# Kernel tuning notes

Hardware: AMD Instinct MI355X
Metric: run time of the kernel (lower is better)

Reference implementation:

```python
import jax, jax.numpy as jnp
import numpy as np
import math

EMSIZE = 512
NX = 2048        # emsize * (layer_id+1), layer_id=3
H = NX // EMSIZE # 4 heads of size EMSIZE (grow_head path)
B, S = 4, 2048
EPS = 1e-5


def _layernorm(x, g, b):
    u = jnp.mean(x, axis=-1, keepdims=True)
    s = jnp.mean((x - u) ** 2, axis=-1, keepdims=True)
    return g * (x - u) / jnp.sqrt(s + EPS) + b


def _gelu(x):
    # OpenAI tanh-approx gelu, exactly as in source
    return 0.5 * x * (1.0 + jnp.tanh(jnp.sqrt(2.0 / jnp.pi) * (x + 0.044715 * x ** 3)))


def setup_inputs() -> dict:
    key = jax.random.key(0)
    ks = jax.random.split(key, 8)
    std = 0.02
    return {
        "x": jax.random.normal(ks[0], (B, S, NX), jnp.float32),
        "w_qkv": jax.random.normal(ks[1], (NX, 3 * NX), jnp.float32) * std,
        "b_qkv": jnp.zeros((3 * NX,), jnp.float32),
        "w_ao": jax.random.normal(ks[2], (NX, NX), jnp.float32) * std,
        "b_ao": jnp.zeros((NX,), jnp.float32),
        "ln1_g": jnp.ones((NX,), jnp.float32),
        "ln1_b": jnp.zeros((NX,), jnp.float32),
        "w_fc": jax.random.normal(ks[3], (NX, 4 * NX), jnp.float32) * std,
        "b_fc": jnp.zeros((4 * NX,), jnp.float32),
        "w_pr": jax.random.normal(ks[4], (4 * NX, NX), jnp.float32) * std,
        "b_pr": jnp.zeros((NX,), jnp.float32),
        "ln2_g": jnp.ones((NX,), jnp.float32),
        "ln2_b": jnp.zeros((NX,), jnp.float32),
        "w_out": jax.random.normal(ks[5], (NX, EMSIZE), jnp.float32) * std,
        "b_out": jnp.zeros((EMSIZE,), jnp.float32),
    }


def reference(x, w_qkv, b_qkv, w_ao, b_ao, ln1_g, ln1_b, w_fc, b_fc,
              w_pr, b_pr, ln2_g, ln2_b, w_out, b_out):
    Bx, Sx, _ = x.shape
    # --- multi-head attention ---
    qkv = x @ w_qkv + b_qkv                       # [B,S,3*NX]
    q, k, v = jnp.split(qkv, 3, axis=-1)
    q = q.reshape(Bx, Sx, H, EMSIZE).transpose(0, 2, 1, 3)  # [B,H,S,E]
    k = k.reshape(Bx, Sx, H, EMSIZE).transpose(0, 2, 1, 3)
    v = v.reshape(Bx, Sx, H, EMSIZE).transpose(0, 2, 1, 3)
    w = jnp.einsum("bhqe,bhke->bhqk", q, k) / jnp.sqrt(jnp.float32(EMSIZE))
    alen = jnp.arange(Sx)
    mask = alen[None, :] <= alen[:, None]          # causal [S,S]
    # source: w*mask + -1e9*(1-mask) == where(mask, w, -1e9)
    w = jnp.where(mask[None, None], w, jnp.float32(-1e9))
    w = jax.nn.softmax(w, axis=-1)
    a = jnp.einsum("bhqk,bhke->bhqe", w, v)        # [B,H,S,E]
    a = a.transpose(0, 2, 1, 3).reshape(Bx, Sx, NX)
    a = a @ w_ao + b_ao
    # --- residual + LN + MLP + LN ---
    n = _layernorm(x + a, ln1_g, ln1_b)
    m = (_gelu(n @ w_fc + b_fc)) @ w_pr + b_pr
    h = _layernorm(n + m, ln2_g, ln2_b)
    # --- final projection + grow_head concat ---
    h = h @ w_out + b_out                          # [B,S,EMSIZE]
    h = h.reshape(Bx, Sx, 1, EMSIZE)
    j = x.reshape(Bx, Sx, H, EMSIZE)
    out = jnp.concatenate([j, h], axis=-2)         # [B,S,H+1,E]
    return out.reshape(Bx, Sx, (H + 1) * EMSIZE)
```

## Files before the change

kernel.cpp:

```cpp
#include <hip/hip_runtime.h>
#include <hip/hip_bf16.h>
#include <math.h>

using bf16 = __hip_bfloat16;
typedef __attribute__((ext_vector_type(8))) short s16x8;
typedef __attribute__((ext_vector_type(4))) float f32x4;

struct __align__(16) B8 { bf16 v[8]; };
struct __align__(8)  B4 { bf16 v[4]; };

__device__ __forceinline__ float b2f(bf16 x){ return __bfloat162float(x); }
__device__ __forceinline__ bf16  f2b(float x){ return __float2bfloat16(x); }

enum { EPI_QKV=0, EPI_AO=3, EPI_FC=4, EPI_PRB=5, EPI_OUT=6 };

#define SCHED0 __builtin_amdgcn_sched_barrier(0)
#define PRIO1  __builtin_amdgcn_s_setprio(1)
#define PRIO0  __builtin_amdgcn_s_setprio(0)
#define BAR    __builtin_amdgcn_s_barrier()
#define VM6    asm volatile("s_waitcnt vmcnt(6)" ::: "memory")
#define VM4    asm volatile("s_waitcnt vmcnt(4)" ::: "memory")
#define VM2    asm volatile("s_waitcnt vmcnt(2)" ::: "memory")
#define VM0    asm volatile("s_waitcnt vmcnt(0)" ::: "memory")
#define LGKM0  asm volatile("s_waitcnt lgkmcnt(0)" ::: "memory")
#define AS1    const __attribute__((address_space(1))) void*
#define AS3    __attribute__((address_space(3))) void*

template<int EPI>
__launch_bounds__(512, 2)
__global__ void gemm256(const bf16* __restrict__ A, const bf16* __restrict__ B,
                        void* __restrict__ Cv, const float* __restrict__ bias,
                        const void* __restrict__ res,
                        int K, int lda, int ldb, int ldc, int ldres, int nbx)
{
    extern __shared__ __align__(16) bf16 lds[];
    bf16* Asl = lds;
    bf16* Bsl = lds + 32768;

    const int nwg = (int)gridDim.x;
    int wg = (int)blockIdx.x;
    if ((nwg & 7) == 0) wg = (wg & 7)*(nwg >> 3) + (wg >> 3);
    const int bx = wg % nbx, by = wg / nbx;
    const long m0 = (long)by*256, n0 = (long)bx*256;

    if constexpr (EPI==EPI_OUT){
        const long ko = (long)blockIdx.y * K;
        A += ko; B += ko;
        Cv = (void*)((float*)Cv + (long)blockIdx.y * 4194304);
    }

    const int tid = threadIdx.x, wave = tid>>6, lane = tid&63;
    const int wr = wave>>2, wc = wave&3;
    const int NT = K>>6;
    const int fr = lane&15, fg = lane>>4;

    const int ck0 = fg ^ (fr&7);
    const int ck1 = (4+fg) ^ (fr&7);
    const bf16* aRd0 = Asl + wr*4096 + fr*64 + ck0*8;
    const bf16* aRd1 = Asl + wr*4096 + fr*64 + ck1*8;
    const bf16* bRd0 = Bsl + wc*2048 + fr*64 + ck0*8;
    const bf16* bRd1 = Bsl + wc*2048 + fr*64 + ck1*8;

    #define RDA(d, rh) { _Pragma("unroll") for (int i=0;i<4;++i){ \
        a[i][0] = *(const s16x8*)(aRd0 + (d)*16384 + (rh)*8192 + i*1024); \
        a[i][1] = *(const s16x8*)(aRd1 + (d)*16384 + (rh)*8192 + i*1024); } }
    #define RDB(dst, d, ch) { _Pragma("unroll") for (int j=0;j<2;++j){ \
        dst[j][0] = *(const s16x8*)(bRd0 + (d)*16384 + (ch)*8192 + j*1024); \
        dst[j][1] = *(const s16x8*)(bRd1 + (d)*16384 + (ch)*8192 + j*1024); } }

    const int grow = tid>>3;
    const int gc0  = (tid&7) ^ (grow&7);
    const bf16* aP = A + (m0 + grow)*(long)lda + gc0*8;
    const bf16* bP = B + (n0 + grow)*(long)ldb + gc0*8;

    #define STGA(sd, sh, koff) { _Pragma("unroll") for (int l=0;l<2;++l) \
        __builtin_amdgcn_global_load_lds((AS1)(aP + ((sh)*128 + l*64)*(long)lda + (koff)), \
            (AS3)(Asl + (sd)*16384 + (sh)*8192 + l*4096 + wave*512 + lane*8), 16, 0, 0); }
    #define STGB(sd, sh, koff) { _Pragma("unroll") for (int l=0;l<2;++l) \
        __builtin_amdgcn_global_load_lds((AS1)(bP + ((sh)*128 + l*64)*(long)ldb + (koff)), \
            (AS3)(Bsl + (sd)*16384 + (sh)*8192 + l*4096 + wave*512 + lane*8), 16, 0, 0); }

    f32x4 acc[2][4][2][2];
    #pragma unroll
    for (int rh=0;rh<2;++rh)
        #pragma unroll
        for (int i=0;i<4;++i)
            #pragma unroll
            for (int ch=0;ch<2;++ch)
                #pragma unroll
                for (int j=0;j<2;++j)
                    #pragma unroll
                    for (int r=0;r<4;++r) acc[rh][i][ch][j][r] = 0.f;

    #define MM(rh, ch, BB) { PRIO1; \
        _Pragma("unroll") for (int i=0;i<4;++i) \
        _Pragma("unroll") for (int j=0;j<2;++j) \
        _Pragma("unroll") for (int kk=0;kk<2;++kk) \
            acc[rh][i][ch][j] = __builtin_amdgcn_mfma_f32_16x16x32_bf16(a[i][kk], BB[j][kk], acc[rh][i][ch][j], 0,0,0); \
        PRIO0; }

    s16x8 a[4][2], b0[2][2], b1[2][2];

    STGA(0,0,0);  STGB(0,1,0);  STGA(0,1,0);  STGB(0,0,0);
    STGA(1,0,64); STGB(1,1,64); STGA(1,1,64);
    VM6; BAR;

    for (int t=0; t<=NT-4; t+=2){
        RDB(b0,0,0); RDA(0,0); STGB(1,0,64);
        BAR; LGKM0; MM(0,0,b0); BAR;
        RDB(b1,0,1);           STGA(0,0,128);
        BAR; LGKM0; MM(0,1,b1); BAR;
        RDA(0,1);              STGB(0,1,128);
        BAR; LGKM0; MM(1,1,b1); BAR;
                               STGA(0,1,128); VM6;
        BAR; LGKM0; MM(1,0,b0); BAR;
        RDB(b0,1,0); RDA(1,0); STGB(0,0,128);
        BAR; LGKM0; MM(0,0,b0); BAR;
        RDB(b1,1,1);           STGA(1,0,192);
        BAR; LGKM0; MM(0,1,b1); BAR;
        RDA(1,1);              STGB(1,1,192);
        BAR; LGKM0; MM(1,1,b1); BAR;
                               STGA(1,1,192); VM6;
        BAR; LGKM0; MM(1,0,b0); BAR;
        aP += 128; bP += 128;
    }

    RDB(b0,0,0); RDA(0,0); STGB(1,0,64);
    BAR; LGKM0; MM(0,0,b0); BAR;
    RDB(b1,0,1);
    BAR; LGKM0; MM(0,1,b1); BAR;
    RDA(0,1);
    BAR; LGKM0; MM(1,1,b1); BAR;
    VM0;
    BAR; LGKM0; MM(1,0,b0); BAR;
    RDB(b0,1,0); RDA(1,0);
    BAR; LGKM0; MM(0,0,b0); BAR;
    RDB(b1,1,1);
    BAR; LGKM0; MM(0,1,b1); BAR;
    RDA(1,1);
    BAR; LGKM0; MM(1,1,b1); BAR;
    MM(1,0,b0);

    #undef RDA
    #undef RDB
    #undef STGA
    #undef STGB
    #undef MM

    #pragma unroll
    for (int rh=0;rh<2;++rh)
        #pragma unroll
        for (int i=0;i<4;++i)
            #pragma unroll
            for (int ch=0;ch<2;++ch)
                #pragma unroll
                for (int j=0;j<2;++j)
                    #pragma unroll
                    for (int r=0;r<4;++r){
                        const long mm = m0 + rh*128 + wr*64 + i*16 + fg*4 + r;
                        const long nn = n0 + ch*128 + wc*32 + j*16 + fr;
                        const float v = acc[rh][i][ch][j][r];
                        if constexpr (EPI==EPI_AO){
                            ((float*)Cv)[mm*ldc + nn] = v + bias[nn] + ((const float*)res)[mm*ldres + nn];
                        } else if constexpr (EPI==EPI_PRB){
                            ((bf16*)Cv)[mm*ldc + nn] = f2b(v + bias[nn] + b2f(((const bf16*)res)[mm*ldres + nn]));
                        } else if constexpr (EPI==EPI_FC){
                            const float tt = v + bias[nn];
                            const float g = 0.5f*tt*(1.f + tanhf(0.7978845608028654f*(tt + 0.044715f*tt*tt*tt)));
                            ((bf16*)Cv)[mm*ldc + nn] = f2b(g);
                        } else if constexpr (EPI==EPI_OUT){
                            ((float*)Cv)[mm*ldc + nn] = v;
                        } else {
                            ((bf16*)Cv)[mm*ldc + nn] = f2b(v + bias[nn]);
                        }
                    }
}

__launch_bounds__(256)
__global__ void kred(const float* __restrict__ p, const float* __restrict__ bias,
                     float* __restrict__ outp){
    const long idx = ((long)blockIdx.x*256 + threadIdx.x)*4;
    const long r = idx>>9, c = idx&511;
    float4 s0 = *(const float4*)&p[idx];
    const float4 s1 = *(const float4*)&p[idx + 4194304];
    const float4 s2 = *(const float4*)&p[idx + 8388608];
    const float4 s3 = *(const float4*)&p[idx + 12582912];
    const float4 bb = *(const float4*)&bias[c];
    s0.x += s1.x+s2.x+s3.x+bb.x; s0.y += s1.y+s2.y+s3.y+bb.y;
    s0.z += s1.z+s2.z+s3.z+bb.z; s0.w += s1.w+s2.w+s3.w+bb.w;
    *(float4*)&outp[r*2560 + 2048 + c] = s0;
}

__launch_bounds__(512, 2)
__global__ void fattn(const bf16* __restrict__ qkv, const bf16* __restrict__ vt,
                      bf16* __restrict__ outp)
{
    extern __shared__ __align__(16) bf16 sh[];
    bf16* sQ = sh;
    bf16* sK = sh + 32768;
    bf16* sP = sh + 57344;
    bf16* sV = sh + 65536;
    float* part = (float*)(sh + 32768);

    const int bid = blockIdx.x;
    const int xcd = bid&7, t5 = bid>>3, rnd = t5>>5, ci = t5&31;
    const int bh = xcd*2 + rnd, b = bh>>2, h = bh&3;
    const int ib = 31 - ci;
    const int njb = (ib>>1) + 1;
    const int tid = threadIdx.x, wave = tid>>6, lane = tid&63;
    const int wr = wave>>2, wc = wave&3;
    const int fr = lane&15, fg = lane>>4;

    const bf16* Qg = qkv + ((long)b*2048 + ib*64)*6144 + h*512;
    const bf16* Kg = qkv + (long)b*2048*6144 + 2048 + h*512;
    const bf16* Vtb = vt + (long)bh*1048576;
    const float SCALE = 0.044194173824159216f;

    #define STGQ { _Pragma("unroll") for (int l=0;l<8;++l){                          \
        const int row = l*8 + (tid>>6);                                              \
        const int c   = (tid&63) ^ (row&7);                                          \
        __builtin_amdgcn_global_load_lds((AS1)(Qg + (long)row*6144 + c*8),           \
            (AS3)(sQ + l*4096 + wave*512 + lane*8), 16,0,0); } }
    #define STGK(slot, ec, KJ) { _Pragma("unroll") for (int l=0;l<2;++l){            \
        const int row = l*64 + (tid>>3);                                             \
        const int c   = (tid&7) ^ (row&7);                                           \
        __builtin_amdgcn_global_load_lds((AS1)((KJ) + (long)row*6144 + (ec)*64 + c*8),\
            (AS3)(sK + (slot)*8192 + l*4096 + wave*512 + lane*8), 16,0,0); } }
    #define STGV(buf, kf, eh, VJ) { _Pragma("unroll") for (int l=0;l<2;++l){         \
        const int row = l*128 + (tid>>2);                                            \
        const int c   = (tid&3) ^ ((row + (row>>2))&3);                              \
        __builtin_amdgcn_global_load_lds((AS1)((VJ) + (long)((eh)*256+row)*2048 + (kf)*32 + c*8),\
            (AS3)(sV + (buf)*8192 + l*4096 + wave*512 + lane*8), 16,0,0); } }

    f32x4 acc[2][8];
    #pragma unroll
    for (int m=0;m<2;++m)
        #pragma unroll
        for (int j=0;j<8;++j)
            #pragma unroll
            for (int r=0;r<4;++r) acc[m][j][r] = 0.f;
    float l_l[2][4];
    #pragma unroll
    for (int m=0;m<2;++m){ l_l[m][0]=0.f; l_l[m][1]=0.f; l_l[m][2]=0.f; l_l[m][3]=0.f; }

    const bf16* KgJ = Kg;
    const bf16* VtJ = Vtb;

    STGQ;
    STGK(0, 0, KgJ);
    STGK(1, 1, KgJ);
    VM2; SCHED0; BAR;

    for (int jb=0; jb<njb; ++jb){
        const bool last = (jb == njb-1);
        f32x4 sacc[2][2];
        #pragma unroll
        for (int m=0;m<2;++m)
            #pragma unroll
            for (int nf=0;nf<2;++nf)
                #pragma unroll
                for (int r=0;r<4;++r) sacc[m][nf][r] = 0.f;

        #pragma unroll
        for (int ec=0; ec<8; ++ec){
            const int slot = ec%3;
            s16x8 qa[2][2], kb[2][2];
            #pragma unroll
            for (int m=0;m<2;++m)
                #pragma unroll
                for (int kk=0;kk<2;++kk){
                    const int row = wr*32 + m*16 + fr;
                    const int c = (ec*2+kk)*4 + fg;
                    qa[m][kk] = *(const s16x8*)(sQ + row*512 + ((c ^ (row&7))*8));
                }
            #pragma unroll
            for (int nf=0;nf<2;++nf)
                #pragma unroll
                for (int kk=0;kk<2;++kk){
                    const int row = wc*32 + nf*16 + fr;
                    const int c = kk*4 + fg;
                    kb[nf][kk] = *(const s16x8*)(sK + slot*8192 + row*64 + ((c ^ (row&7))*8));
                }
            if (ec < 6) STGK((ec+2)%3, ec+2, KgJ);
            PRIO1;
            #pragma unroll
            for (int m=0;m<2;++m)
                #pragma unroll
                for (int nf=0;nf<2;++nf)
                    #pragma unroll
                    for (int kk=0;kk<2;++kk)
                        sacc[m][nf] = __builtin_amdgcn_mfma_f32_16x16x32_bf16(qa[m][kk], kb[nf][kk], sacc[m][nf], 0,0,0);
            PRIO0;
            if (ec < 6) { VM2; } else if (ec == 6) { VM0; }
            SCHED0; BAR;
        }

        const int doff = (njb-1)*128 - ib*64;
        #pragma unroll
        for (int m=0;m<2;++m)
            #pragma unroll
            for (int nf=0;nf<2;++nf)
                #pragma unroll
                for (int r=0;r<4;++r){
                    float pv = __expf(sacc[m][nf][r]*SCALE - 4.0f);
                    const int rl = wr*32 + m*16 + fg*4 + r;
                    const int cl = wc*32 + nf*16 + fr;
                    if (last && (cl + doff > rl)) pv = 0.f;
                    sP[rl*128 + (((cl>>3) ^ (rl&15))*8) + (cl&7)] = f2b(pv);
                    l_l[m][r] += pv;
                }
        STGV(0, 0, 0, VtJ);
        if (!last){ STGK(0, 0, KgJ + 786432); STGK(1, 1, KgJ + 786432); }
        if (!last){ VM4; } else { VM0; }
        LGKM0; SCHED0; BAR;

        s16x8 pa[2];
        #pragma unroll
        for (int v=0; v<8; ++v){
            const int kf = v>>1, eh = v&1, buf = v&1;
            if (eh == 0){
                #pragma unroll
                for (int m=0;m<2;++m){
                    const int row = wr*32 + m*16 + fr;
                    const int c = kf*4 + fg;
                    pa[m] = *(const s16x8*)(sP + row*128 + ((c ^ (row&15))*8));
                }
            }
            s16x8 vb[4];
            #pragma unroll
            for (int nf=0;nf<4;++nf){
                const int row = wc*64 + nf*16 + fr;
                vb[nf] = *(const s16x8*)(sV + buf*8192 + row*32 + (((fg ^ ((row + (row>>2))&3)))*8));
            }
            if (v < 7) STGV((v+1)&1, (v+1)>>1, (v+1)&1, VtJ);
            PRIO1;
            #pragma unroll
            for (int m=0;m<2;++m)
                #pragma unroll
                for (int nf=0;nf<4;++nf)
                    acc[m][eh*4+nf] = __builtin_amdgcn_mfma_f32_16x16x32_bf16(pa[m], vb[nf], acc[m][eh*4+nf], 0,0,0);
            PRIO0;
            if (v < 7) { VM0; }
            SCHED0; BAR;
        }
        KgJ += 786432;
        VtJ += 128;
    }

    #pragma unroll
    for (int m=0;m<2;++m)
        #pragma unroll
        for (int r=0;r<4;++r){
            float v = l_l[m][r];
            v += __shfl_xor(v, 1); v += __shfl_xor(v, 2);
            v += __shfl_xor(v, 4); v += __shfl_xor(v, 8);
            l_l[m][r] = v;
        }
    if (fr == 0){
        #pragma unroll
        for (int m=0;m<2;++m)
            #pragma unroll
            for (int r=0;r<4;++r)
                part[(wr*32 + m*16 + fg*4 + r)*4 + wc] = l_l[m][r];
    }
    LGKM0; SCHED0; BAR;

    bf16* orow = outp + ((long)b*2048 + ib*64)*2048 + h*512;
    #pragma unroll
    for (int m=0;m<2;++m)
        #pragma unroll
        for (int r=0;r<4;++r){
            const int rl = wr*32 + m*16 + fg*4 + r;
            const f32x4 pp = *(const f32x4*)(part + rl*4);
            const float rinv = 1.f/(pp[0]+pp[1]+pp[2]+pp[3]);
            #pragma unroll
            for (int j=0;j<8;++j){
                const int e = (j>>2)*256 + wc*64 + (j&3)*16 + fr;
                orow[(long)rl*2048 + e] = f2b(acc[m][j][r]*rinv);
            }
        }
    #undef STGQ
    #undef STGK
    #undef STGV
}

__launch_bounds__(256)
__global__ void wtrans(const float* __restrict__ W, bf16* __restrict__ Wt, int Kd, int Nd){
    __shared__ float t[32][33];
    const int n0 = blockIdx.x*32, k0 = blockIdx.y*32;
    const int tx = threadIdx.x&31, ty = threadIdx.x>>5;
    #pragma unroll
    for (int i=0;i<32;i+=8) t[ty+i][tx] = W[(long)(k0+ty+i)*Nd + n0+tx];
    __syncthreads();
    #pragma unroll
    for (int i=0;i<32;i+=8) Wt[(long)(n0+ty+i)*Kd + k0+tx] = f2b(t[tx][ty+i]);
}

__launch_bounds__(256)
__global__ void vtrans(const bf16* __restrict__ qkv, bf16* __restrict__ vt){
    const int z = blockIdx.z, b = z>>2, h = z&3;
    const bf16* in = qkv + (long)b*12582912 + 4096 + h*512;
    bf16* outp = vt + (long)z*1048576;
    __shared__ bf16 t[32][33];
    const int e0 = blockIdx.x*32, s0 = blockIdx.y*32;
    const int tx = threadIdx.x&31, ty = threadIdx.x>>5;
    #pragma unroll
    for (int i=0;i<32;i+=8) t[ty+i][tx] = in[(long)(s0+ty+i)*6144 + e0+tx];
    __syncthreads();
    #pragma unroll
    for (int i=0;i<32;i+=8) outp[(long)(e0+ty+i)*2048 + s0+tx] = t[tx][ty+i];
}

__launch_bounds__(256)
__global__ void cvt_f32_bf16(const float* __restrict__ in, bf16* __restrict__ outp){
    const long i = ((long)blockIdx.x*256 + threadIdx.x)*4;
    const float4 v = *(const float4*)&in[i];
    B4 o; o.v[0]=f2b(v.x); o.v[1]=f2b(v.y); o.v[2]=f2b(v.z); o.v[3]=f2b(v.w);
    *reinterpret_cast<B4*>(&outp[i]) = o;
}

__launch_bounds__(256)
__global__ void jcopy(const float* __restrict__ x, float* __restrict__ outp){
    const long idx = ((long)blockIdx.x*256 + threadIdx.x)*4;
    const long r = idx>>11, c = idx&2047;
    *(float4*)&outp[r*2560 + c] = *(const float4*)&x[idx];
}

template<int BF>
__launch_bounds__(256)
__global__ void ln_rows(const void* __restrict__ inp, const float* __restrict__ gw,
                        const float* __restrict__ bw, bf16* __restrict__ outp){
    const long r = blockIdx.x;
    const int tid = threadIdx.x, k0 = tid*8;
    float v[8];
    if constexpr (BF){
        const bf16* row = (const bf16*)inp + r*2048;
        const B8 x = *reinterpret_cast<const B8*>(&row[k0]);
        #pragma unroll
        for (int i=0;i<8;++i) v[i] = b2f(x.v[i]);
    } else {
        const float* row = (const float*)inp + r*2048;
        const float4 a = *(const float4*)&row[k0];
        const float4 c = *(const float4*)&row[k0+4];
        v[0]=a.x; v[1]=a.y; v[2]=a.z; v[3]=a.w; v[4]=c.x; v[5]=c.y; v[6]=c.z; v[7]=c.w;
    }
    float s = 0.f, qq = 0.f;
    #pragma unroll
    for (int i=0;i<8;++i){ s += v[i]; qq += v[i]*v[i]; }
    #pragma unroll
    for (int o=32;o;o>>=1){ s += __shfl_xor(s,o); qq += __shfl_xor(qq,o); }
    __shared__ float s1[4], s2[4];
    if ((tid&63)==0){ s1[tid>>6]=s; s2[tid>>6]=qq; }
    __syncthreads();
    s  = s1[0]+s1[1]+s1[2]+s1[3];
    qq = s2[0]+s2[1]+s2[2]+s2[3];
    const float mean = s*(1.f/2048.f);
    const float var  = qq*(1.f/2048.f) - mean*mean;
    const float rinv = rsqrtf(var + 1e-5f);
    const float4 g1 = *(const float4*)&gw[k0];
    const float4 g2 = *(const float4*)&gw[k0+4];
    const float4 b1 = *(const float4*)&bw[k0];
    const float4 b2 = *(const float4*)&bw[k0+4];
    const float gg[8] = {g1.x,g1.y,g1.z,g1.w,g2.x,g2.y,g2.z,g2.w};
    const float bb[8] = {b1.x,b1.y,b1.z,b1.w,b2.x,b2.y,b2.z,b2.w};
    B8 o;
    #pragma unroll
    for (int i=0;i<8;++i) o.v[i] = f2b((v[i]-mean)*rinv*gg[i] + bb[i]);
    *reinterpret_cast<B8*>(&outp[r*2048 + k0]) = o;
}

extern "C" void kernel_launch(void* const* d_in, const int* in_sizes, int n_in,
                              void* d_out, int out_size, void* d_ws, size_t ws_size,
                              hipStream_t stream)
{
    (void)in_sizes; (void)n_in; (void)out_size;
    const float* x     = (const float*)d_in[0];
    const float* w_qkv = (const float*)d_in[1];
    const float* b_qkv = (const float*)d_in[2];
    const float* w_ao  = (const float*)d_in[3];
    const float* b_ao  = (const float*)d_in[4];
    const float* ln1g  = (const float*)d_in[5];
    const float* ln1b  = (const float*)d_in[6];
    const float* w_fc  = (const float*)d_in[7];
    const float* b_fc  = (const float*)d_in[8];
    const float* w_pr  = (const float*)d_in[9];
    const float* b_pr  = (const float*)d_in[10];
    const float* ln2g  = (const float*)d_in[11];
    const float* ln2b  = (const float*)d_in[12];
    const float* w_out = (const float*)d_in[13];
    const float* b_out = (const float*)d_in[14];
    float* out = (float*)d_out;
    char* ws = (char*)d_ws;

    const size_t NEEDED = 245366784ull;
    if (ws_size < NEEDED) return;

    bf16*  xb     = (bf16*)(ws);
    bf16*  qkv    = (bf16*)(ws + 33554432ull);
    float* r1     = (float*)(ws + 33554432ull);
    bf16*  fcact  = (bf16*)(ws);
    float* kpart  = (float*)(ws);
    bf16*  vt     = (bf16*)(ws + 134217728ull);
    bf16*  Wfc_t  = (bf16*)(ws + 134217728ull);
    bf16*  rbufB  = (bf16*)(ws + 134217728ull);
    bf16*  Wpr_t  = (bf16*)(ws + 167772160ull);
    bf16*  Wqkv_t = (bf16*)(ws + 201326592ull);
    bf16*  nbuf   = (bf16*)(ws + 201326592ull);
    bf16*  Wao_t  = (bf16*)(ws + 234881024ull);
    bf16*  Wout_t = (bf16*)(ws + 243269632ull);

    const dim3 T(256);
    const int SMEM = 131072;
    const int SMEM_A = 163840;
    (void)hipFuncSetAttribute((const void*)gemm256<EPI_QKV>, hipFuncAttributeMaxDynamicSharedMemorySize, SMEM);
    (void)hipFuncSetAttribute((const void*)gemm256<EPI_AO>,  hipFuncAttributeMaxDynamicSharedMemorySize, SMEM);
    (void)hipFuncSetAttribute((const void*)gemm256<EPI_FC>,  hipFuncAttributeMaxDynamicSharedMemorySize, SMEM);
    (void)hipFuncSetAttribute((const void*)gemm256<EPI_PRB>, hipFuncAttributeMaxDynamicSharedMemorySize, SMEM);
    (void)hipFuncSetAttribute((const void*)gemm256<EPI_OUT>, hipFuncAttributeMaxDynamicSharedMemorySize, SMEM);
    (void)hipFuncSetAttribute((const void*)fattn,            hipFuncAttributeMaxDynamicSharedMemorySize, SMEM_A);

    wtrans<<<dim3(192,64),T,0,stream>>>(w_qkv, Wqkv_t, 2048, 6144);
    wtrans<<<dim3(64,64), T,0,stream>>>(w_ao,  Wao_t,  2048, 2048);
    wtrans<<<dim3(16,64), T,0,stream>>>(w_out, Wout_t, 2048, 512);
    cvt_f32_bf16<<<16384,T,0,stream>>>(x, xb);

    gemm256<EPI_QKV><<<dim3(768),dim3(512),SMEM,stream>>>(xb, Wqkv_t, qkv, b_qkv, nullptr,
        2048, 2048, 2048, 6144, 0, 24);
    vtrans<<<dim3(16,64,16),T,0,stream>>>(qkv, vt);

    fattn<<<dim3(512),dim3(512),SMEM_A,stream>>>(qkv, vt, xb);

    gemm256<EPI_AO><<<dim3(256),dim3(512),SMEM,stream>>>(xb, Wao_t, r1, b_ao, x,
        2048, 2048, 2048, 2048, 2048, 8);
    ln_rows<0><<<8192,T,0,stream>>>(r1, ln1g, ln1b, nbuf);

    wtrans<<<dim3(256,64),T,0,stream>>>(w_fc, Wfc_t, 2048, 8192);
    wtrans<<<dim3(64,256),T,0,stream>>>(w_pr, Wpr_t, 8192, 2048);
    gemm256<EPI_FC><<<dim3(1024),dim3(512),SMEM,stream>>>(nbuf, Wfc_t, fcact, b_fc, nullptr,
        2048, 2048, 2048, 8192, 0, 32);
    gemm256<EPI_PRB><<<dim3(256),dim3(512),SMEM,stream>>>(fcact, Wpr_t, rbufB, b_pr, nbuf,
        8192, 8192, 8192, 2048, 2048, 8);
    ln_rows<1><<<8192,T,0,stream>>>(rbufB, ln2g, ln2b, nbuf);

    gemm256<EPI_OUT><<<dim3(64,4),dim3(512),SMEM,stream>>>(nbuf, Wout_t, kpart, nullptr, nullptr,
        512, 2048, 2048, 512, 0, 2);
    kred<<<4096,T,0,stream>>>(kpart, b_out, out);
    jcopy<<<16384,T,0,stream>>>(x, out);
}
```

Measured before the change: 1.065 ms.

## Fuse V transpose into QKV epilogue, merge x conversion and copy, bf16 AO output

The QKV GEMM epilogue now writes the V columns straight into the transposed per-head layout, so the separate vtrans kernel goes away. The x-to-bf16 conversion and the passthrough copy into the output are merged into one kernel that reads x once. The attention-output GEMM now stores its residual sum as bf16 instead of fp32, which halves that buffer's traffic before layernorm, at some cost in precision. The transposed V stores are 8-byte writes strided by 2048, which may coalesce poorly.

```diff
diff --git a/kernel.cpp b/kernel.cpp
--- a/kernel.cpp
+++ b/kernel.cpp
@@ -147,33 +147,54 @@
     #undef STGB
     #undef MM
 
+    const bool vmode = (n0 >= 4096);
+    bf16* vtp = (bf16*)res;
     #pragma unroll
     for (int rh=0;rh<2;++rh)
         #pragma unroll
-        for (int i=0;i<4;++i)
+        for (int i=0;i<4;++i){
+            const long mmb = m0 + rh*128 + wr*64 + i*16 + fg*4;
             #pragma unroll
             for (int ch=0;ch<2;++ch)
                 #pragma unroll
-                for (int j=0;j<2;++j)
-                    #pragma unroll
-                    for (int r=0;r<4;++r){
-                        const long mm = m0 + rh*128 + wr*64 + i*16 + fg*4 + r;
-                        const long nn = n0 + ch*128 + wc*32 + j*16 + fr;
-                        const float v = acc[rh][i][ch][j][r];
-                        if constexpr (EPI==EPI_AO){
-                            ((float*)Cv)[mm*ldc + nn] = v + bias[nn] + ((const float*)res)[mm*ldres + nn];
-                        } else if constexpr (EPI==EPI_PRB){
-                            ((bf16*)Cv)[mm*ldc + nn] = f2b(v + bias[nn] + b2f(((const bf16*)res)[mm*ldres + nn]));
-                        } else if constexpr (EPI==EPI_FC){
-                            const float tt = v + bias[nn];
+                for (int j=0;j<2;++j){
+                    const long nn = n0 + ch*128 + wc*32 + j*16 + fr;
+                    if constexpr (EPI==EPI_QKV){
+                        if (vmode){
+                            B4 o;
+                            #pragma unroll
+                            for (int r=0;r<4;++r) o.v[r] = f2b(acc[rh][i][ch][j][r] + bias[nn]);
+                            *reinterpret_cast<B4*>(vtp + (((mmb>>11)<<2) + ((nn-4096)>>9))*1048576
+                                                   + (nn&511)*2048 + (mmb&2047)) = o;
+                        } else {
+                            #pragma unroll
+                            for (int r=0;r<4;++r)
+                                ((bf16*)Cv)[(mmb+r)*ldc + nn] = f2b(acc[rh][i][ch][j][r] + bias[nn]);
+                        }
+                    } else if constexpr (EPI==EPI_AO){
+                        #pragma unroll
+                        for (int r=0;r<4;++r)
+                            ((bf16*)Cv)[(mmb+r)*ldc + nn] =
+                                f2b(acc[rh][i][ch][j][r] + bias[nn] + ((const float*)res)[(mmb+r)*ldres + nn]);
+                    } else if constexpr (EPI==EPI_PRB){
+                        #pragma unroll
+                        for (int r=0;r<4;++r)
+                            ((bf16*)Cv)[(mmb+r)*ldc + nn] =
+                                f2b(acc[rh][i][ch][j][r] + bias[nn] + b2f(((const bf16*)res)[(mmb+r)*ldres + nn]));
+                    } else if constexpr (EPI==EPI_FC){
+                        #pragma unroll
+                        for (int r=0;r<4;++r){
+                            const float tt = acc[rh][i][ch][j][r] + bias[nn];
                             const float g = 0.5f*tt*(1.f + tanhf(0.7978845608028654f*(tt + 0.044715f*tt*tt*tt)));
-                            ((bf16*)Cv)[mm*ldc + nn] = f2b(g);
-                        } else if constexpr (EPI==EPI_OUT){
-                            ((float*)Cv)[mm*ldc + nn] = v;
-                        } else {
-                            ((bf16*)Cv)[mm*ldc + nn] = f2b(v + bias[nn]);
+                            ((bf16*)Cv)[(mmb+r)*ldc + nn] = f2b(g);
                         }
+                    } else {
+                        #pragma unroll
+                        for (int r=0;r<4;++r)
+                            ((float*)Cv)[(mmb+r)*ldc + nn] = acc[rh][i][ch][j][r];
                     }
+                }
+        }
 }
 
 __launch_bounds__(256)
@@ -397,33 +418,14 @@
 }
 
 __launch_bounds__(256)
-__global__ void vtrans(const bf16* __restrict__ qkv, bf16* __restrict__ vt){
-    const int z = blockIdx.z, b = z>>2, h = z&3;
-    const bf16* in = qkv + (long)b*12582912 + 4096 + h*512;
-    bf16* outp = vt + (long)z*1048576;
-    __shared__ bf16 t[32][33];
-    const int e0 = blockIdx.x*32, s0 = blockIdx.y*32;
-    const int tx = threadIdx.x&31, ty = threadIdx.x>>5;
-    #pragma unroll
-    for (int i=0;i<32;i+=8) t[ty+i][tx] = in[(long)(s0+ty+i)*6144 + e0+tx];
-    __syncthreads();
-    #pragma unroll
-    for (int i=0;i<32;i+=8) outp[(long)(e0+ty+i)*2048 + s0+tx] = t[tx][ty+i];
-}
-
-__launch_bounds__(256)
-__global__ void cvt_f32_bf16(const float* __restrict__ in, bf16* __restrict__ outp){
-    const long i = ((long)blockIdx.x*256 + threadIdx.x)*4;
-    const float4 v = *(const float4*)&in[i];
+__global__ void xprep(const float* __restrict__ x, bf16* __restrict__ xb,
+                      float* __restrict__ outp){
+    const long idx = ((long)blockIdx.x*256 + threadIdx.x)*4;
+    const float4 v = *(const float4*)&x[idx];
     B4 o; o.v[0]=f2b(v.x); o.v[1]=f2b(v.y); o.v[2]=f2b(v.z); o.v[3]=f2b(v.w);
-    *reinterpret_cast<B4*>(&outp[i]) = o;
-}
-
-__launch_bounds__(256)
-__global__ void jcopy(const float* __restrict__ x, float* __restrict__ outp){
-    const long idx = ((long)blockIdx.x*256 + threadIdx.x)*4;
+    *reinterpret_cast<B4*>(&xb[idx]) = o;
     const long r = idx>>11, c = idx&2047;
-    *(float4*)&outp[r*2560 + c] = *(const float4*)&x[idx];
+    *(float4*)&outp[r*2560 + c] = v;
 }
 
 template<int BF>
@@ -497,7 +499,7 @@
 
     bf16*  xb     = (bf16*)(ws);
     bf16*  qkv    = (bf16*)(ws + 33554432ull);
-    float* r1     = (float*)(ws + 33554432ull);
+    bf16*  r1b    = (bf16*)(ws + 33554432ull);
     bf16*  fcact  = (bf16*)(ws);
     float* kpart  = (float*)(ws);
     bf16*  vt     = (bf16*)(ws + 134217728ull);
@@ -522,17 +524,16 @@
     wtrans<<<dim3(192,64),T,0,stream>>>(w_qkv, Wqkv_t, 2048, 6144);
     wtrans<<<dim3(64,64), T,0,stream>>>(w_ao,  Wao_t,  2048, 2048);
     wtrans<<<dim3(16,64), T,0,stream>>>(w_out, Wout_t, 2048, 512);
-    cvt_f32_bf16<<<16384,T,0,stream>>>(x, xb);
-
-    gemm256<EPI_QKV><<<dim3(768),dim3(512),SMEM,stream>>>(xb, Wqkv_t, qkv, b_qkv, nullptr,
+    xprep<<<16384,T,0,stream>>>(x, xb, out);
+
+    gemm256<EPI_QKV><<<dim3(768),dim3(512),SMEM,stream>>>(xb, Wqkv_t, qkv, b_qkv, vt,
         2048, 2048, 2048, 6144, 0, 24);
-    vtrans<<<dim3(16,64,16),T,0,stream>>>(qkv, vt);
 
     fattn<<<dim3(512),dim3(512),SMEM_A,stream>>>(qkv, vt, xb);
 
-    gemm256<EPI_AO><<<dim3(256),dim3(512),SMEM,stream>>>(xb, Wao_t, r1, b_ao, x,
+    gemm256<EPI_AO><<<dim3(256),dim3(512),SMEM,stream>>>(xb, Wao_t, r1b, b_ao, x,
         2048, 2048, 2048, 2048, 2048, 8);
-    ln_rows<0><<<8192,T,0,stream>>>(r1, ln1g, ln1b, nbuf);
+    ln_rows<1><<<8192,T,0,stream>>>(r1b, ln1g, ln1b, nbuf);
 
     wtrans<<<dim3(256,64),T,0,stream>>>(w_fc, Wfc_t, 2048, 8192);
     wtrans<<<dim3(64,256),T,0,stream>>>(w_pr, Wpr_t, 8192, 2048);
@@ -545,5 +546,4 @@
     gemm256<EPI_OUT><<<dim3(64,4),dim3(512),SMEM,stream>>>(nbuf, Wout_t, kpart, nullptr, nullptr,
         512, 2048, 2048, 512, 0, 2);
     kred<<<4096,T,0,stream>>>(kpart, b_out, out);
-    jcopy<<<16384,T,0,stream>>>(x, out);
-}
+}
```

Measured after the change: 1.050 ms. About the same (-1.4%).
